# Kernel tuning notes

Hardware: AMD Instinct MI355X
Metric: run time of the kernel (lower is better)

The kernel has to match this reference:

```python
import jax, jax.numpy as jnp
import numpy as np

GRID_SIZE = 5
GRID_RANGE = (-1.0, 1.0)


def setup_inputs() -> dict:
    key = jax.random.key(0)
    k1, k2, k3 = jax.random.split(key, 3)
    B, D, U, K = 16384, 1024, 128, GRID_SIZE + 3  # spline_order=3
    x = jax.random.normal(k1, (B, D), dtype=jnp.float32)
    # glorot-ish scale for weights
    base_weight = jax.random.normal(k2, (D, U), dtype=jnp.float32) * (1.0 / np.sqrt(D))
    spline_weight = jax.random.normal(k3, (D, U, K), dtype=jnp.float32) * (1.0 / np.sqrt(D))
    return {"x": x, "base_weight": base_weight, "spline_weight": spline_weight}


def reference(x, base_weight, spline_weight):
    # base path: SiLU(x @ W_b)
    base_out = jax.nn.silu(x @ base_weight)  # [B, U]
    # spline path: RBF over grid centers, then contract (note: x_norm in the
    # original call() is computed but unused, so it is omitted here)
    centers = jnp.linspace(GRID_RANGE[0], GRID_RANGE[1], GRID_SIZE)  # [G]
    dist = jnp.square(x[..., None] - centers)        # [B, D, G]
    rbf = jnp.exp(-5.0 * dist)                        # [B, D, G]
    spline_out = jnp.einsum('big,iug->bu', rbf, spline_weight[:, :, :GRID_SIZE])
    return base_out + spline_out
```

## Files before the change

kernel.cpp:

```cpp
#include <hip/hip_runtime.h>

typedef unsigned short u16;
typedef unsigned int u32;
typedef __bf16 bf16x8 __attribute__((ext_vector_type(8)));
typedef float f32x16 __attribute__((ext_vector_type(16)));

#define C2 (-7.213475204444817f)
#define T1C 0.28650480f
#define T2C 0.0067379470f

__device__ __forceinline__ u16 f2bf(float f) {
  u32 u = __float_as_uint(f);
  return (u16)((u + 0x7FFFu + ((u >> 16) & 1u)) >> 16);
}

__device__ __forceinline__ f32x16 mfma16(uint4 a, uint4 b, f32x16 c) {
  return __builtin_amdgcn_mfma_f32_32x32x16_bf16(
      __builtin_bit_cast(bf16x8, a), __builtin_bit_cast(bf16x8, b), c, 0, 0, 0);
}

__global__ __launch_bounds__(256) void kan_prep(const float* __restrict__ wb,
                                                const float* __restrict__ ws,
                                                u16* __restrict__ wst3) {
  __shared__ u16 tile[6][16][130];
  const int t = threadIdx.x;
  const int c = blockIdx.x;
#pragma unroll
  for (int it = 0; it < 8; ++it) {
    int idx = it * 256 + t;
    int d = idx >> 7, u = idx & 127;
    size_t base = (size_t)(c * 16 + d) * 128 + u;
    const float* p = ws + base * 8;
    float4 v0 = *(const float4*)p;
    float g4 = p[4];
    tile[0][d][u] = f2bf(v0.x);
    tile[1][d][u] = f2bf(v0.y);
    tile[2][d][u] = f2bf(v0.z);
    tile[3][d][u] = f2bf(v0.w);
    tile[4][d][u] = f2bf(g4);
    tile[5][d][u] = f2bf(wb[base]);
  }
  __syncthreads();
#pragma unroll
  for (int i = 0; i < 6; ++i) {
    int g = i * 256 + t;
    int s = g >> 8, r = g & 255;
    int nq = r >> 6, l = r & 63;
    int u = nq * 32 + (l & 31);
    int dbase = (l >> 5) * 8;
    u32 q[4];
#pragma unroll
    for (int j = 0; j < 4; ++j) {
      u32 lo = tile[s][dbase + 2 * j][u];
      u32 hi = tile[s][dbase + 2 * j + 1][u];
      q[j] = lo | (hi << 16);
    }
    uint4 w4; w4.x = q[0]; w4.y = q[1]; w4.z = q[2]; w4.w = q[3];
    *(uint4*)(wst3 + (size_t)c * 12288 + (size_t)g * 8) = w4;
  }
}

__global__ __launch_bounds__(512, 2) void kan_main(const float* __restrict__ x,
                                                   const u16* __restrict__ wst3,
                                                   float* __restrict__ out) {
  __shared__ __align__(16) char lds[98304];

  const int t = threadIdx.x;
  const int lane = t & 63;
  const int w = t >> 6;
  const int kq = w & 3;
  const int wn = w >> 2;
  const int b0 = blockIdx.x * 64;

  f32x16 acc[8];
#pragma unroll
  for (int i = 0; i < 8; ++i)
#pragma unroll
    for (int j = 0; j < 16; ++j) acc[i][j] = 0.f;

  const int r = t >> 3, o = t & 7;
  const float* xp = x + (size_t)(b0 + r) * 1024 + o * 8;
  const u32 aw = (u32)((((r >> 5) * 4 + (o >> 1)) << 10) + ((o & 1) << 9) +
                       (((r & 31) ^ o) << 4));

  const char* bsrc = (const char*)wst3 + kq * 24576 + wn * 2048 + lane * 16;

  const u32 ar = (u32)((kq << 10) + ((lane >> 5) << 9) +
                       ((((lane & 31) ^ (kq * 2 + (lane >> 5)))) << 4));

  auto rbf_write = [&](char* buf, float4 xa, float4 xb) {
    float xf[8] = {xa.x, xa.y, xa.z, xa.w, xb.x, xb.y, xb.z, xb.w};
    u32 pk[6][4];
#pragma unroll
    for (int pp = 0; pp < 4; ++pp) {
      u32 lo6[6], hi6[6];
#pragma unroll
      for (int e = 0; e < 2; ++e) {
        float xv = xf[2 * pp + e];
        float t0 = C2 * xv;
        float P = __builtin_amdgcn_exp2f(t0 * xv);
        float Qp = __builtin_amdgcn_exp2f(-t0);
        float Qm = __builtin_amdgcn_exp2f(t0);
        float PQ = P * Qp, PQm = P * Qm;
        u32* dst = e ? hi6 : lo6;
        dst[0] = __float_as_uint(PQm * Qm * T2C) + 0x8000u;
        dst[1] = __float_as_uint(PQm * T1C) + 0x8000u;
        dst[2] = __float_as_uint(P) + 0x8000u;
        dst[3] = __float_as_uint(PQ * T1C) + 0x8000u;
        dst[4] = __float_as_uint(PQ * Qp * T2C) + 0x8000u;
        dst[5] = __float_as_uint(xv) + 0x8000u;
      }
#pragma unroll
      for (int s = 0; s < 6; ++s)
        pk[s][pp] = __builtin_amdgcn_perm(hi6[s], lo6[s], 0x07060302);
    }
#pragma unroll
    for (int s = 0; s < 6; ++s) {
      uint4 v; v.x = pk[s][0]; v.y = pk[s][1]; v.z = pk[s][2]; v.w = pk[s][3];
      *(uint4*)(buf + s * 8192 + aw) = v;
    }
  };

  float4 xc0 = *(const float4*)(xp);
  float4 xc1 = *(const float4*)(xp + 4);
  rbf_write(lds, xc0, xc1);
  xc0 = *(const float4*)(xp + 64);
  xc1 = *(const float4*)(xp + 68);
  __syncthreads();

  for (int i = 0; i < 16; ++i) {
    char* cur = lds + (size_t)(i & 1) * 49152;
    char* nxt = lds + (size_t)((i + 1) & 1) * 49152;
    const char* bc = bsrc + (size_t)i * 98304;

    uint4 av[6], bv[6];
#pragma unroll
    for (int s = 0; s < 3; ++s) {
      bv[2 * s] = *(const uint4*)(bc + s * 4096);
      bv[2 * s + 1] = *(const uint4*)(bc + s * 4096 + 1024);
      av[2 * s] = *(const uint4*)(cur + s * 8192 + ar);
      av[2 * s + 1] = *(const uint4*)(cur + s * 8192 + 4096 + ar);
    }
    if (i < 15) {
      rbf_write(nxt, xc0, xc1);
      if (i < 14) {
        xc0 = *(const float4*)(xp + (i + 2) * 64);
        xc1 = *(const float4*)(xp + (i + 2) * 64 + 4);
      }
    }
#pragma unroll
    for (int s = 0; s < 3; ++s) {
      acc[0] = mfma16(av[2 * s], bv[2 * s], acc[0]);
      acc[1] = mfma16(av[2 * s], bv[2 * s + 1], acc[1]);
      acc[2] = mfma16(av[2 * s + 1], bv[2 * s], acc[2]);
      acc[3] = mfma16(av[2 * s + 1], bv[2 * s + 1], acc[3]);
    }
#pragma unroll
    for (int s = 3; s < 6; ++s) {
      int j = 2 * (s - 3);
      bv[j] = *(const uint4*)(bc + s * 4096);
      bv[j + 1] = *(const uint4*)(bc + s * 4096 + 1024);
      av[j] = *(const uint4*)(cur + s * 8192 + ar);
      av[j + 1] = *(const uint4*)(cur + s * 8192 + 4096 + ar);
    }
#pragma unroll
    for (int s = 3; s < 5; ++s) {
      int j = 2 * (s - 3);
      acc[0] = mfma16(av[j], bv[j], acc[0]);
      acc[1] = mfma16(av[j], bv[j + 1], acc[1]);
      acc[2] = mfma16(av[j + 1], bv[j], acc[2]);
      acc[3] = mfma16(av[j + 1], bv[j + 1], acc[3]);
    }
    acc[4] = mfma16(av[4], bv[4], acc[4]);
    acc[5] = mfma16(av[4], bv[5], acc[5]);
    acc[6] = mfma16(av[5], bv[4], acc[6]);
    acc[7] = mfma16(av[5], bv[5], acc[7]);
    __syncthreads();
  }

#pragma unroll
  for (int q = 0; q < 4; ++q) {
    if (kq != 0) {
      char* slab = lds + ((kq - 1) * 2 + wn) * 8192;
#pragma unroll
      for (int rq = 0; rq < 4; ++rq) {
        *(float4*)(slab + rq * 1024 + lane * 16) =
            make_float4(acc[q][4 * rq], acc[q][4 * rq + 1],
                        acc[q][4 * rq + 2], acc[q][4 * rq + 3]);
        *(float4*)(slab + 4096 + rq * 1024 + lane * 16) =
            make_float4(acc[4 + q][4 * rq], acc[4 + q][4 * rq + 1],
                        acc[4 + q][4 * rq + 2], acc[4 + q][4 * rq + 3]);
      }
    }
    __syncthreads();
    if (kq == 0) {
#pragma unroll
      for (int p = 1; p < 4; ++p) {
        const char* slab = lds + ((p - 1) * 2 + wn) * 8192;
#pragma unroll
        for (int rq = 0; rq < 4; ++rq) {
          float4 vs = *(const float4*)(slab + rq * 1024 + lane * 16);
          float4 vb = *(const float4*)(slab + 4096 + rq * 1024 + lane * 16);
          acc[q][4 * rq] += vs.x; acc[q][4 * rq + 1] += vs.y;
          acc[q][4 * rq + 2] += vs.z; acc[q][4 * rq + 3] += vs.w;
          acc[4 + q][4 * rq] += vb.x; acc[4 + q][4 * rq + 1] += vb.y;
          acc[4 + q][4 * rq + 2] += vb.z; acc[4 + q][4 * rq + 3] += vb.w;
        }
      }
      const int col = wn * 64 + (q & 1) * 32 + (lane & 31);
#pragma unroll
      for (int reg = 0; reg < 16; ++reg) {
        int row = (q >> 1) * 32 + (reg & 3) + 8 * (reg >> 2) + 4 * (lane >> 5);
        float z = acc[4 + q][reg];
        float sv = z / (1.0f + __expf(-z));
        out[(size_t)(b0 + row) * 128 + col] = sv + acc[q][reg];
      }
    }
    __syncthreads();
  }
}

extern "C" void kernel_launch(void* const* d_in, const int* in_sizes, int n_in,
                              void* d_out, int out_size, void* d_ws, size_t ws_size,
                              hipStream_t stream) {
  const float* x  = (const float*)d_in[0];
  const float* wb = (const float*)d_in[1];
  const float* ws = (const float*)d_in[2];
  u16* wst3 = (u16*)d_ws;
  float* out = (float*)d_out;

  kan_prep<<<dim3(64), 256, 0, stream>>>(wb, ws, wst3);
  kan_main<<<dim3(256), 512, 0, stream>>>(x, wst3, out);
}
```

Measured before the change: 136.6 us.

## Double wave count per block, halving per-wave N tile and accumulators

```diff
diff --git a/kernel.cpp b/kernel.cpp
--- a/kernel.cpp
+++ b/kernel.cpp
@@ -60,39 +60,42 @@
   }
 }
 
-__global__ __launch_bounds__(512, 2) void kan_main(const float* __restrict__ x,
-                                                   const u16* __restrict__ wst3,
-                                                   float* __restrict__ out) {
+__global__ __launch_bounds__(1024, 4) void kan_main(const float* __restrict__ x,
+                                                    const u16* __restrict__ wst3,
+                                                    float* __restrict__ out) {
   __shared__ __align__(16) char lds[98304];
 
   const int t = threadIdx.x;
   const int lane = t & 63;
   const int w = t >> 6;
-  const int kq = w & 3;
-  const int wn = w >> 2;
+  const int wn = w & 3;
+  const int kq = w >> 2;
   const int b0 = blockIdx.x * 64;
 
-  f32x16 acc[8];
-#pragma unroll
-  for (int i = 0; i < 8; ++i)
+  f32x16 acc[4];
+#pragma unroll
+  for (int i = 0; i < 4; ++i)
 #pragma unroll
     for (int j = 0; j < 16; ++j) acc[i][j] = 0.f;
 
-  const int r = t >> 3, o = t & 7;
-  const float* xp = x + (size_t)(b0 + r) * 1024 + o * 8;
-  const u32 aw = (u32)((((r >> 5) * 4 + (o >> 1)) << 10) + ((o & 1) << 9) +
-                       (((r & 31) ^ o) << 4));
-
-  const char* bsrc = (const char*)wst3 + kq * 24576 + wn * 2048 + lane * 16;
-
-  const u32 ar = (u32)((kq << 10) + ((lane >> 5) << 9) +
-                       ((((lane & 31) ^ (kq * 2 + (lane >> 5)))) << 4));
-
-  auto rbf_write = [&](char* buf, float4 xa, float4 xb) {
-    float xf[8] = {xa.x, xa.y, xa.z, xa.w, xb.x, xb.y, xb.z, xb.w};
-    u32 pk[6][4];
-#pragma unroll
-    for (int pp = 0; pp < 4; ++pp) {
+  const int r = w * 4 + (t & 3);
+  const int q4 = (t >> 2) & 15;
+  const float* xp = x + (size_t)(b0 + r) * 1024 + q4 * 4;
+  const int kqw = q4 >> 2, khw = (q4 >> 1) & 1, half = q4 & 1;
+  const u32 aw = (u32)((r >> 5) * 4096 + kqw * 1024 + khw * 512 +
+                       (((r & 31) ^ (kqw * 2 + khw)) << 4) + half * 8);
+
+  const char* bsrc = (const char*)wst3 + kq * 24576 + wn * 1024 + lane * 16;
+
+  const int kh = lane >> 5;
+  const u32 ar = (u32)(kq * 1024 + kh * 512 +
+                       (((lane & 31) ^ (kq * 2 + kh)) << 4));
+
+  auto rbf_write = [&](char* buf, float4 xa) {
+    float xf[4] = {xa.x, xa.y, xa.z, xa.w};
+    u32 pk[6][2];
+#pragma unroll
+    for (int pp = 0; pp < 2; ++pp) {
       u32 lo6[6], hi6[6];
 #pragma unroll
       for (int e = 0; e < 2; ++e) {
@@ -116,16 +119,14 @@
     }
 #pragma unroll
     for (int s = 0; s < 6; ++s) {
-      uint4 v; v.x = pk[s][0]; v.y = pk[s][1]; v.z = pk[s][2]; v.w = pk[s][3];
-      *(uint4*)(buf + s * 8192 + aw) = v;
+      uint2 v; v.x = pk[s][0]; v.y = pk[s][1];
+      *(uint2*)(buf + s * 8192 + aw) = v;
     }
   };
 
-  float4 xc0 = *(const float4*)(xp);
-  float4 xc1 = *(const float4*)(xp + 4);
-  rbf_write(lds, xc0, xc1);
-  xc0 = *(const float4*)(xp + 64);
-  xc1 = *(const float4*)(xp + 68);
+  float4 xc = *(const float4*)(xp);
+  rbf_write(lds, xc);
+  xc = *(const float4*)(xp + 64);
   __syncthreads();
 
   for (int i = 0; i < 16; ++i) {
@@ -133,87 +134,76 @@
     char* nxt = lds + (size_t)((i + 1) & 1) * 49152;
     const char* bc = bsrc + (size_t)i * 98304;
 
-    uint4 av[6], bv[6];
+    uint4 av[6], bv[3];
 #pragma unroll
     for (int s = 0; s < 3; ++s) {
-      bv[2 * s] = *(const uint4*)(bc + s * 4096);
-      bv[2 * s + 1] = *(const uint4*)(bc + s * 4096 + 1024);
+      bv[s] = *(const uint4*)(bc + s * 4096);
       av[2 * s] = *(const uint4*)(cur + s * 8192 + ar);
       av[2 * s + 1] = *(const uint4*)(cur + s * 8192 + 4096 + ar);
     }
     if (i < 15) {
-      rbf_write(nxt, xc0, xc1);
-      if (i < 14) {
-        xc0 = *(const float4*)(xp + (i + 2) * 64);
-        xc1 = *(const float4*)(xp + (i + 2) * 64 + 4);
-      }
+      rbf_write(nxt, xc);
+      if (i < 14) xc = *(const float4*)(xp + (i + 2) * 64);
     }
 #pragma unroll
     for (int s = 0; s < 3; ++s) {
-      acc[0] = mfma16(av[2 * s], bv[2 * s], acc[0]);
-      acc[1] = mfma16(av[2 * s], bv[2 * s + 1], acc[1]);
-      acc[2] = mfma16(av[2 * s + 1], bv[2 * s], acc[2]);
-      acc[3] = mfma16(av[2 * s + 1], bv[2 * s + 1], acc[3]);
+      acc[0] = mfma16(av[2 * s], bv[s], acc[0]);
+      acc[1] = mfma16(av[2 * s + 1], bv[s], acc[1]);
     }
 #pragma unroll
     for (int s = 3; s < 6; ++s) {
       int j = 2 * (s - 3);
-      bv[j] = *(const uint4*)(bc + s * 4096);
-      bv[j + 1] = *(const uint4*)(bc + s * 4096 + 1024);
+      bv[s - 3] = *(const uint4*)(bc + s * 4096);
       av[j] = *(const uint4*)(cur + s * 8192 + ar);
       av[j + 1] = *(const uint4*)(cur + s * 8192 + 4096 + ar);
     }
 #pragma unroll
     for (int s = 3; s < 5; ++s) {
       int j = 2 * (s - 3);
-      acc[0] = mfma16(av[j], bv[j], acc[0]);
-      acc[1] = mfma16(av[j], bv[j + 1], acc[1]);
-      acc[2] = mfma16(av[j + 1], bv[j], acc[2]);
-      acc[3] = mfma16(av[j + 1], bv[j + 1], acc[3]);
-    }
-    acc[4] = mfma16(av[4], bv[4], acc[4]);
-    acc[5] = mfma16(av[4], bv[5], acc[5]);
-    acc[6] = mfma16(av[5], bv[4], acc[6]);
-    acc[7] = mfma16(av[5], bv[5], acc[7]);
+      acc[0] = mfma16(av[j], bv[s - 3], acc[0]);
+      acc[1] = mfma16(av[j + 1], bv[s - 3], acc[1]);
+    }
+    acc[2] = mfma16(av[4], bv[2], acc[2]);
+    acc[3] = mfma16(av[5], bv[2], acc[3]);
     __syncthreads();
   }
 
 #pragma unroll
-  for (int q = 0; q < 4; ++q) {
+  for (int g = 0; g < 2; ++g) {
     if (kq != 0) {
-      char* slab = lds + ((kq - 1) * 2 + wn) * 8192;
+      char* slab = lds + ((kq - 1) * 4 + wn) * 8192;
 #pragma unroll
       for (int rq = 0; rq < 4; ++rq) {
         *(float4*)(slab + rq * 1024 + lane * 16) =
-            make_float4(acc[q][4 * rq], acc[q][4 * rq + 1],
-                        acc[q][4 * rq + 2], acc[q][4 * rq + 3]);
+            make_float4(acc[g][4 * rq], acc[g][4 * rq + 1],
+                        acc[g][4 * rq + 2], acc[g][4 * rq + 3]);
         *(float4*)(slab + 4096 + rq * 1024 + lane * 16) =
-            make_float4(acc[4 + q][4 * rq], acc[4 + q][4 * rq + 1],
-                        acc[4 + q][4 * rq + 2], acc[4 + q][4 * rq + 3]);
+            make_float4(acc[2 + g][4 * rq], acc[2 + g][4 * rq + 1],
+                        acc[2 + g][4 * rq + 2], acc[2 + g][4 * rq + 3]);
       }
     }
     __syncthreads();
     if (kq == 0) {
 #pragma unroll
       for (int p = 1; p < 4; ++p) {
-        const char* slab = lds + ((p - 1) * 2 + wn) * 8192;
+        const char* slab = lds + ((p - 1) * 4 + wn) * 8192;
 #pragma unroll
         for (int rq = 0; rq < 4; ++rq) {
           float4 vs = *(const float4*)(slab + rq * 1024 + lane * 16);
           float4 vb = *(const float4*)(slab + 4096 + rq * 1024 + lane * 16);
-          acc[q][4 * rq] += vs.x; acc[q][4 * rq + 1] += vs.y;
-          acc[q][4 * rq + 2] += vs.z; acc[q][4 * rq + 3] += vs.w;
-          acc[4 + q][4 * rq] += vb.x; acc[4 + q][4 * rq + 1] += vb.y;
-          acc[4 + q][4 * rq + 2] += vb.z; acc[4 + q][4 * rq + 3] += vb.w;
+          acc[g][4 * rq] += vs.x; acc[g][4 * rq + 1] += vs.y;
+          acc[g][4 * rq + 2] += vs.z; acc[g][4 * rq + 3] += vs.w;
+          acc[2 + g][4 * rq] += vb.x; acc[2 + g][4 * rq + 1] += vb.y;
+          acc[2 + g][4 * rq + 2] += vb.z; acc[2 + g][4 * rq + 3] += vb.w;
         }
       }
-      const int col = wn * 64 + (q & 1) * 32 + (lane & 31);
+      const int col = wn * 32 + (lane & 31);
 #pragma unroll
       for (int reg = 0; reg < 16; ++reg) {
-        int row = (q >> 1) * 32 + (reg & 3) + 8 * (reg >> 2) + 4 * (lane >> 5);
-        float z = acc[4 + q][reg];
+        int row = g * 32 + (reg & 3) + 8 * (reg >> 2) + 4 * (lane >> 5);
+        float z = acc[2 + g][reg];
         float sv = z / (1.0f + __expf(-z));
-        out[(size_t)(b0 + row) * 128 + col] = sv + acc[q][reg];
+        out[(size_t)(b0 + row) * 128 + col] = sv + acc[g][reg];
       }
     }
     __syncthreads();
@@ -230,5 +220,5 @@
   float* out = (float*)d_out;
 
   kan_prep<<<dim3(64), 256, 0, stream>>>(wb, ws, wst3);
-  kan_main<<<dim3(256), 512, 0, stream>>>(x, wst3, out);
-}
+  kan_main<<<dim3(256), 1024, 0, stream>>>(x, wst3, out);
+}
```

After: 139.6 us. 1.02x slower.
